# Performance work log

Measured on AMD Instinct MI355X. Metric: run time of the kernel, lower is better.

The kernel has to match this reference:

```python
import jax, jax.numpy as jnp
import numpy as np

B, C, H, W = 4, 384, 128, 128
HEADS = 8
EPS = 1e-12  # torch F.normalize default eps


def setup_inputs() -> dict:
    key = jax.random.key(0)
    k1, k2, k3, k4 = jax.random.split(key, 4)
    in1 = jax.random.normal(k1, (B, C, H, W), dtype=jnp.float32)
    in2 = jax.random.normal(k2, (B, C, H, W), dtype=jnp.float32)
    temperature = jnp.ones((HEADS, 1, 1), dtype=jnp.float32)
    proj_w = jax.random.normal(k3, (C, C), dtype=jnp.float32) * (1.0 / np.sqrt(C))
    proj_b = jax.random.normal(k4, (C,), dtype=jnp.float32) * 0.01
    return {"in1": in1, "in2": in2, "temperature": temperature,
            "proj_w": proj_w, "proj_b": proj_b}


def _l2norm_last(x):
    # torch F.normalize(dim=-1): x / max(||x||_2, eps)
    n = jnp.sqrt(jnp.sum(x * x, axis=-1, keepdims=True))
    return x / jnp.maximum(n, EPS)


def reference(in1, in2, temperature, proj_w, proj_b):
    b, c, h, w = in1.shape
    hd = c // HEADS  # per-head channels
    # b (head c) h w -> b head c (h w)
    q = in1.reshape(b, HEADS, hd, h * w)
    k = in2.reshape(b, HEADS, hd, h * w)
    q = _l2norm_last(q)
    k = _l2norm_last(k)
    # channel attention: [b, head, hd, hd]
    attn = jnp.einsum('bhcn,bhdn->bhcd', q, k) * temperature[None]
    attn = jax.nn.softmax(attn, axis=-1)
    out = jnp.einsum('bhcd,bhdn->bhcn', attn, k)  # [b, head, hd, HW]
    out = out.reshape(b, c, h, w)
    # 1x1 conv projection
    out = jnp.einsum('oc,bchw->bohw', proj_w, out) + proj_b[None, :, None, None]
    return out
```

## Files before the change

### kernel.cpp

```cpp
#include <hip/hip_runtime.h>
#include <hip/hip_bf16.h>

#define NB 4
#define CC 384
#define HEADS 8
#define HD 48
#define NN 16384
#define NROWS (NB*CC)

typedef __attribute__((ext_vector_type(8))) short bf16x8;
typedef __attribute__((ext_vector_type(4))) float f32x4;

__device__ __forceinline__ unsigned short f2bf(float f) {
  __hip_bfloat16 h = __float2bfloat16(f);
  return __builtin_bit_cast(unsigned short, h);
}
__device__ __forceinline__ unsigned int packbf(float a, float b) {
  return (unsigned int)f2bf(a) | ((unsigned int)f2bf(b) << 16);
}
__device__ __forceinline__ float bf2f(short s) {
  unsigned int u = ((unsigned int)(unsigned short)s) << 16;
  return __builtin_bit_cast(float, u);
}

#define SROW 264
__global__ __launch_bounds__(256) void k_gram(
    const float* __restrict__ in1, const float* __restrict__ in2,
    float* __restrict__ partial, float* __restrict__ sumsq_part)
{
  int bh = blockIdx.x;
  int chunk = blockIdx.y;
  int wave = threadIdx.x >> 6, lane = threadIdx.x & 63;
  int b = bh >> 3, h = bh & 7;
  size_t base = ((size_t)(b*CC + h*HD)) * NN;
  int lrow = lane & 15, lkg = lane >> 4;

  __shared__ char smem[50688];
  unsigned short* sq_ = (unsigned short*)smem;
  unsigned short* sk_ = (unsigned short*)(smem + 25344);
  float* red = (float*)smem;
  float* sqs = (float*)(smem + 38400);

  f32x4 acc[3][3] = {};
  float ssq[3] = {0.f,0.f,0.f}, ssk[3] = {0.f,0.f,0.f};

  for (int rnd = 0; rnd < 2; ++rnd) {
    int kbase = chunk*512 + rnd*256;
    #pragma unroll 8
    for (int rr = 0; rr < 24; ++rr) {
      int row = wave*24 + rr;
      int tr = row < 48 ? row : row - 48;
      const float* src = (row < 48 ? in1 : in2) + base + (size_t)tr*NN + kbase;
      float4 v = *(const float4*)(src + lane*4);
      unsigned short* dstp = (row < 48 ? sq_ : sk_) + tr*SROW + lane*4;
      *(unsigned int*)(dstp)     = packbf(v.x, v.y);
      *(unsigned int*)(dstp + 2) = packbf(v.z, v.w);
    }
    __syncthreads();
    #pragma unroll
    for (int ks = 0; ks < 2; ++ks) {
      int col = wave*64 + ks*32 + lkg*8;
      bf16x8 a[3], bb[3];
      #pragma unroll
      for (int t = 0; t < 3; ++t) {
        int rr2 = t*16 + lrow;
        a[t]  = *(const bf16x8*)(sq_ + rr2*SROW + col);
        bb[t] = *(const bf16x8*)(sk_ + rr2*SROW + col);
      }
      #pragma unroll
      for (int t = 0; t < 3; ++t)
        #pragma unroll
        for (int j = 0; j < 8; ++j) {
          float fa = bf2f(a[t][j]);  ssq[t] += fa*fa;
          float fb = bf2f(bb[t][j]); ssk[t] += fb*fb;
        }
      #pragma unroll
      for (int i = 0; i < 3; ++i)
        #pragma unroll
        for (int j = 0; j < 3; ++j)
          acc[i][j] = __builtin_amdgcn_mfma_f32_16x16x32_bf16(a[i], bb[j], acc[i][j], 0, 0, 0);
    }
    __syncthreads();
  }

  #pragma unroll
  for (int i = 0; i < 3; ++i)
    #pragma unroll
    for (int j = 0; j < 3; ++j)
      #pragma unroll
      for (int m = 0; m < 4; ++m) {
        int rr2 = i*16 + (lane>>4)*4 + m;
        int cc2 = j*16 + (lane&15);
        red[(size_t)wave*2400 + rr2*50 + cc2] = acc[i][j][m];
      }
  #pragma unroll
  for (int t = 0; t < 3; ++t) {
    float s = ssq[t]; s += __shfl_xor(s, 16); s += __shfl_xor(s, 32);
    if (lane < 16) sqs[wave*96 + t*16 + lane] = s;
    float s2 = ssk[t]; s2 += __shfl_xor(s2, 16); s2 += __shfl_xor(s2, 32);
    if (lane < 16) sqs[wave*96 + 48 + t*16 + lane] = s2;
  }
  __syncthreads();
  float* pout = partial + ((size_t)bh*32 + chunk) * (HD*HD);
  for (int e = threadIdx.x; e < HD*HD; e += 256) {
    int r = e / HD, c = e % HD;
    pout[e] = red[r*50+c] + red[2400 + r*50+c] + red[4800 + r*50+c] + red[7200 + r*50+c];
  }
  if (threadIdx.x < 96) {
    float* sout = sumsq_part + ((size_t)bh*32 + chunk) * 96;
    sout[threadIdx.x] = sqs[threadIdx.x] + sqs[96 + threadIdx.x]
                      + sqs[192 + threadIdx.x] + sqs[288 + threadIdx.x];
  }
}

__global__ __launch_bounds__(256) void k_redsm(
    const float* __restrict__ partial, const float* __restrict__ sumsq_part,
    const float* __restrict__ temp, float* __restrict__ attn_out,
    float* __restrict__ rinv_k_g)
{
  int bh = blockIdx.x; int b = bh >> 3, h = bh & 7;
  __shared__ float attn[HD][HD+1];
  __shared__ float rqs[HD], rks[HD];
  if (threadIdx.x < 96) {
    float s = 0.f;
    #pragma unroll
    for (int c = 0; c < 32; ++c)
      s += sumsq_part[((size_t)bh*32 + c)*96 + threadIdx.x];
    float rinv = 1.f / fmaxf(sqrtf(s), 1e-12f);
    if (threadIdx.x < 48) rqs[threadIdx.x] = rinv;
    else { rks[threadIdx.x-48] = rinv; rinv_k_g[b*CC + h*HD + threadIdx.x-48] = rinv; }
  }
  const float* p = partial + (size_t)bh * 32 * (HD*HD);
  float tscale = temp[h];
  __syncthreads();
  for (int e = threadIdx.x; e < HD*HD; e += 256) {
    float s = 0.f;
    #pragma unroll
    for (int c2 = 0; c2 < 32; ++c2) s += p[c2*(HD*HD) + e];
    attn[e/HD][e%HD] = s * tscale * rqs[e/HD] * rks[e%HD];
  }
  __syncthreads();
  if (threadIdx.x < HD) {
    float* rowp = attn[threadIdx.x];
    float m = rowp[0];
    for (int j = 1; j < HD; ++j) m = fmaxf(m, rowp[j]);
    float sum = 0.f;
    for (int j = 0; j < HD; ++j) { float e = expf(rowp[j]-m); rowp[j] = e; sum += e; }
    float inv = 1.f / sum;
    for (int j = 0; j < HD; ++j) rowp[j] *= inv;
  }
  __syncthreads();
  float* ao = attn_out + (size_t)bh * (HD*HD);
  for (int e = threadIdx.x; e < HD*HD; e += 256)
    ao[e] = attn[e/HD][e%HD];
}

__global__ __launch_bounds__(256) void k_m(
    const float* __restrict__ attn, const float* __restrict__ proj_w,
    const float* __restrict__ rinv_k, unsigned short* __restrict__ Mbf)
{
  int b = blockIdx.x, ot = blockIdx.y;
  int o0 = ot * 16;
  __shared__ float sw[16*CC];
  __shared__ float sa[HEADS*HD*HD];
  const float* ab = attn + (size_t)b * HEADS * HD * HD;
  for (int i = threadIdx.x; i < HEADS*HD*HD; i += 256) sa[i] = ab[i];
  for (int i = threadIdx.x; i < 16*CC; i += 256)
    sw[i] = proj_w[(size_t)(o0 + i/CC)*CC + (i%CC)];
  __syncthreads();
  for (int idx = threadIdx.x; idx < 16*96; idx += 256) {
    int o = idx / 96, c4 = idx % 96;
    int col = c4 * 4;
    int h = col / HD, d = col % HD;
    const float* wp = sw + o*CC + h*HD;
    const float* ap = sa + h*HD*HD + d;
    f32x4 s = {0.f, 0.f, 0.f, 0.f};
    #pragma unroll
    for (int c2 = 0; c2 < HD; ++c2) {
      float w = wp[c2];
      f32x4 av = *(const f32x4*)(ap + c2*HD);
      s += w * av;
    }
    f32x4 rk = *(const f32x4*)(rinv_k + b*CC + col);
    s *= rk;
    ushort4 o4;
    o4.x = f2bf(s[0]); o4.y = f2bf(s[1]); o4.z = f2bf(s[2]); o4.w = f2bf(s[3]);
    *(ushort4*)(Mbf + ((size_t)b*CC + o0 + o)*CC + col) = o4;
  }
}

#define BM 128
#define BN 128
#define BK 64

__global__ __launch_bounds__(256) void k_final(
    const float* __restrict__ in2, const unsigned short* __restrict__ Mbf,
    const float* __restrict__ bias, float* __restrict__ out)
{
  int b = blockIdx.z;
  int bm = blockIdx.y * BM, bn = blockIdx.x * BN;
  int tid = threadIdx.x, lane = tid & 63, wave = tid >> 6;
  int wrow = wave >> 1, wcol = wave & 1;
  __shared__ unsigned short Bt[BN * BK];
  char* btb = (char*)Bt;
  const float* kb = in2 + (size_t)b * CC * NN;
  const unsigned short* Mb = Mbf + (size_t)b * CC * CC;
  f32x4 acc[4][4] = {};
  int lrow = lane & 15, lkg = lane >> 4;
  for (int k0 = 0; k0 < CC; k0 += BK) {
    #pragma unroll
    for (int s = 0; s < 2; ++s) {
      int slot = tid + s*256;
      int cp = slot >> 4;
      int ng = slot & 15;
      int n0 = ng * 8;
      int c = k0 + cp*2;
      const float* p0 = kb + (size_t)c*NN + bn + n0;
      const float* p1 = kb + (size_t)(c+1)*NN + bn + n0;
      float4 a0 = *(const float4*)p0, a1 = *((const float4*)p0 + 1);
      float4 b0 = *(const float4*)p1, b1 = *((const float4*)p1 + 1);
      float lo[8] = {a0.x,a0.y,a0.z,a0.w,a1.x,a1.y,a1.z,a1.w};
      float hi[8] = {b0.x,b0.y,b0.z,b0.w,b1.x,b1.y,b1.z,b1.w};
      #pragma unroll
      for (int i = 0; i < 8; ++i) {
        int n = n0 + i;
        unsigned int val = packbf(lo[i], hi[i]);
        int pc = (cp>>2) ^ (n & 7) ^ ((n >> 3) & 7);
        *(unsigned int*)(btb + n*128 + (pc<<4) + ((cp&3)<<2)) = val;
      }
    }
    __syncthreads();
    #pragma unroll
    for (int kk = 0; kk < BK; kk += 32) {
      bf16x8 af[4], bfr[4];
      #pragma unroll
      for (int t = 0; t < 4; ++t) {
        int o = bm + wrow*64 + t*16 + lrow;
        af[t] = *(const bf16x8*)(Mb + (size_t)o*CC + (k0 + kk + (lkg<<3)));
        int n = wcol*64 + t*16 + lrow;
        int lc = (kk>>3) + lkg;
        int pc = lc ^ (n & 7) ^ ((n >> 3) & 7);
        bfr[t] = *(const bf16x8*)(btb + n*128 + (pc<<4));
      }
      #pragma unroll
      for (int i = 0; i < 4; ++i)
        #pragma unroll
        for (int j = 0; j < 4; ++j)
          acc[i][j] = __builtin_amdgcn_mfma_f32_16x16x32_bf16(af[i], bfr[j], acc[i][j], 0, 0, 0);
    }
    __syncthreads();
  }
  #pragma unroll
  for (int i = 0; i < 4; ++i) {
    int obase = bm + wrow*64 + i*16 + lkg*4;
    #pragma unroll
    for (int j = 0; j < 4; ++j) {
      int n = bn + wcol*64 + j*16 + lrow;
      #pragma unroll
      for (int m = 0; m < 4; ++m) {
        int o = obase + m;
        out[((size_t)b*CC + o)*NN + n] = acc[i][j][m] + bias[o];
      }
    }
  }
}

extern "C" void kernel_launch(void* const* d_in, const int* in_sizes, int n_in,
                              void* d_out, int out_size, void* d_ws, size_t ws_size,
                              hipStream_t stream)
{
  const float* in1    = (const float*)d_in[0];
  const float* in2    = (const float*)d_in[1];
  const float* temp   = (const float*)d_in[2];
  const float* proj_w = (const float*)d_in[3];
  const float* proj_b = (const float*)d_in[4];
  float* out = (float*)d_out;
  char* ws = (char*)d_ws;

  size_t off = 0;
  float* partial    = (float*)(ws + off); off += (size_t)32*32*HD*HD*4;
  float* sumsq_part = (float*)(ws + off); off += (size_t)32*32*96*4;
  float* attn_out   = (float*)(ws + off); off += (size_t)32*HD*HD*4;
  float* rinv_k     = (float*)(ws + off); off += NROWS*4;
  unsigned short* Mbf = (unsigned short*)(ws + off);

  k_gram<<<dim3(32, 32), dim3(256), 0, stream>>>(in1, in2, partial, sumsq_part);
  k_redsm<<<dim3(32), dim3(256), 0, stream>>>(partial, sumsq_part, temp, attn_out, rinv_k);
  k_m<<<dim3(NB, 24), dim3(256), 0, stream>>>(attn_out, proj_w, rinv_k, Mbf);
  k_final<<<dim3(NN/BN, CC/BM, NB), dim3(256), 0, stream>>>(in2, Mbf, proj_b, out);
}
```

Measured before the change: 130.2 us.

## Halve k_gram shared memory with smaller staging tiles and two-stage reduction

The gram kernel now stages 128 columns per round over four rounds instead of 256 over two, shrinking the bf16 staging buffers. The cross-wave accumulator reduction writes two buffers and adds the other waves in a second step behind an extra barrier, instead of four separate buffers. Together these roughly halve the shared memory per block so more blocks can be resident per CU to hide global load latency. In exchange there are more __syncthreads per block and less MFMA work between barriers.

```diff
diff --git a/kernel.cpp b/kernel.cpp
--- a/kernel.cpp
+++ b/kernel.cpp
@@ -23,7 +23,7 @@
   return __builtin_bit_cast(float, u);
 }
 
-#define SROW 264
+#define SROW2 136
 __global__ __launch_bounds__(256) void k_gram(
     const float* __restrict__ in1, const float* __restrict__ in2,
     float* __restrict__ partial, float* __restrict__ sumsq_part)
@@ -35,37 +35,40 @@
   size_t base = ((size_t)(b*CC + h*HD)) * NN;
   int lrow = lane & 15, lkg = lane >> 4;
 
-  __shared__ char smem[50688];
+  __shared__ char smem[26112];
   unsigned short* sq_ = (unsigned short*)smem;
-  unsigned short* sk_ = (unsigned short*)(smem + 25344);
-  float* red = (float*)smem;
-  float* sqs = (float*)(smem + 38400);
+  unsigned short* sk_ = (unsigned short*)(smem + 13056);
+  float* red2 = (float*)smem;
+  float* sqs  = (float*)(smem + 19200);
 
   f32x4 acc[3][3] = {};
   float ssq[3] = {0.f,0.f,0.f}, ssk[3] = {0.f,0.f,0.f};
 
-  for (int rnd = 0; rnd < 2; ++rnd) {
-    int kbase = chunk*512 + rnd*256;
-    #pragma unroll 8
-    for (int rr = 0; rr < 24; ++rr) {
-      int row = wave*24 + rr;
+  int r2 = lane >> 5;
+  int c4 = (lane & 31) * 4;
+
+  for (int rnd = 0; rnd < 4; ++rnd) {
+    int kbase = chunk*512 + rnd*128;
+    #pragma unroll
+    for (int stp = 0; stp < 12; ++stp) {
+      int row = wave*24 + stp*2 + r2;
       int tr = row < 48 ? row : row - 48;
-      const float* src = (row < 48 ? in1 : in2) + base + (size_t)tr*NN + kbase;
-      float4 v = *(const float4*)(src + lane*4);
-      unsigned short* dstp = (row < 48 ? sq_ : sk_) + tr*SROW + lane*4;
-      *(unsigned int*)(dstp)     = packbf(v.x, v.y);
-      *(unsigned int*)(dstp + 2) = packbf(v.z, v.w);
+      const float* src = (row < 48 ? in1 : in2) + base + (size_t)tr*NN + kbase + c4;
+      float4 v = *(const float4*)src;
+      uint2 pk2;
+      pk2.x = packbf(v.x, v.y);
+      pk2.y = packbf(v.z, v.w);
+      *(uint2*)((row < 48 ? sq_ : sk_) + tr*SROW2 + c4) = pk2;
     }
     __syncthreads();
-    #pragma unroll
-    for (int ks = 0; ks < 2; ++ks) {
-      int col = wave*64 + ks*32 + lkg*8;
+    {
+      int col = wave*32 + lkg*8;
       bf16x8 a[3], bb[3];
       #pragma unroll
       for (int t = 0; t < 3; ++t) {
         int rr2 = t*16 + lrow;
-        a[t]  = *(const bf16x8*)(sq_ + rr2*SROW + col);
-        bb[t] = *(const bf16x8*)(sk_ + rr2*SROW + col);
+        a[t]  = *(const bf16x8*)(sq_ + rr2*SROW2 + col);
+        bb[t] = *(const bf16x8*)(sk_ + rr2*SROW2 + col);
       }
       #pragma unroll
       for (int t = 0; t < 3; ++t)
@@ -83,16 +86,19 @@
     __syncthreads();
   }
 
-  #pragma unroll
-  for (int i = 0; i < 3; ++i)
-    #pragma unroll
-    for (int j = 0; j < 3; ++j)
-      #pragma unroll
-      for (int m = 0; m < 4; ++m) {
-        int rr2 = i*16 + (lane>>4)*4 + m;
-        int cc2 = j*16 + (lane&15);
-        red[(size_t)wave*2400 + rr2*50 + cc2] = acc[i][j][m];
-      }
+  if (wave == 1 || wave == 3) {
+    float* rd = red2 + (wave>>1)*2400;
+    #pragma unroll
+    for (int i = 0; i < 3; ++i)
+      #pragma unroll
+      for (int j = 0; j < 3; ++j)
+        #pragma unroll
+        for (int m = 0; m < 4; ++m) {
+          int rr2 = i*16 + (lane>>4)*4 + m;
+          int cc2 = j*16 + (lane&15);
+          rd[rr2*50 + cc2] = acc[i][j][m];
+        }
+  }
   #pragma unroll
   for (int t = 0; t < 3; ++t) {
     float s = ssq[t]; s += __shfl_xor(s, 16); s += __shfl_xor(s, 32);
@@ -101,10 +107,24 @@
     if (lane < 16) sqs[wave*96 + 48 + t*16 + lane] = s2;
   }
   __syncthreads();
+  if (wave == 0 || wave == 2) {
+    float* rd = red2 + (wave>>1)*2400;
+    #pragma unroll
+    for (int i = 0; i < 3; ++i)
+      #pragma unroll
+      for (int j = 0; j < 3; ++j)
+        #pragma unroll
+        for (int m = 0; m < 4; ++m) {
+          int rr2 = i*16 + (lane>>4)*4 + m;
+          int cc2 = j*16 + (lane&15);
+          rd[rr2*50 + cc2] += acc[i][j][m];
+        }
+  }
+  __syncthreads();
   float* pout = partial + ((size_t)bh*32 + chunk) * (HD*HD);
   for (int e = threadIdx.x; e < HD*HD; e += 256) {
     int r = e / HD, c = e % HD;
-    pout[e] = red[r*50+c] + red[2400 + r*50+c] + red[4800 + r*50+c] + red[7200 + r*50+c];
+    pout[e] = red2[r*50+c] + red2[2400 + r*50+c];
   }
   if (threadIdx.x < 96) {
     float* sout = sumsq_part + ((size_t)bh*32 + chunk) * 96;
```

After: 135.5 us. 4.1% more time.
